# Optimization experiments

Hardware: AMD Instinct MI355X
Metric: run time of the kernel (lower is better)

## Reference

```python
import jax, jax.numpy as jnp
import numpy as np

B, T, P, N, D, H = 4, 8, 32, 64, 256, 8
M = 4 * D  # mlp hidden
EPS_LN = 1e-5


def _layernorm(x, g, b):
    mu = jnp.mean(x, axis=-1, keepdims=True)
    var = jnp.mean(jnp.square(x - mu), axis=-1, keepdims=True)
    return (x - mu) * jax.lax.rsqrt(var + EPS_LN) * g + b


def _attention(y, qkv_w, qkv_b, proj_w, proj_b, bias=None):
    # y: [Bb, Nn, D]; bias broadcastable to [Bb, H, Nn, Nn]
    Bb, Nn, Dd = y.shape
    hd = Dd // H
    qkv = (y @ qkv_w + qkv_b).reshape(Bb, Nn, 3, H, hd)
    qkv = jnp.transpose(qkv, (2, 0, 3, 1, 4))  # [3, Bb, H, Nn, hd]
    q, k, v = qkv[0], qkv[1], qkv[2]
    s = jnp.einsum('bhnd,bhmd->bhnm', q, k) * (hd ** -0.5)
    if bias is not None:
        s = s + bias
    a = jax.nn.softmax(s, axis=-1)
    o = jnp.einsum('bhnm,bhmd->bhnd', a, v)
    o = jnp.transpose(o, (0, 2, 1, 3)).reshape(Bb, Nn, Dd)
    return o @ proj_w + proj_b


def _mlp(y, fc1_w, fc1_b, fc2_w, fc2_b):
    h = jax.nn.gelu(y @ fc1_w + fc1_b, approximate=False)
    return h @ fc2_w + fc2_b


def setup_inputs():
    key = jax.random.key(0)
    ks = jax.random.split(key, 12)
    lin = lambda k, i, o: (jax.random.normal(k, (i, o), jnp.float32) * (i ** -0.5))
    inp = {}
    inp['x'] = jax.random.normal(ks[0], (B, T, P * N, D), jnp.float32)
    inp['mask'] = jax.random.bernoulli(ks[1], 0.8, (P, N)).astype(jnp.float32)
    inp['patch_adj'] = jax.random.uniform(ks[2], (N, N), jnp.float32, minval=0.01, maxval=1.0)
    inp['dn1_g'] = jnp.ones((D,)); inp['dn1_b'] = jnp.zeros((D,))
    inp['dn2_g'] = jnp.ones((D,)); inp['dn2_b'] = jnp.zeros((D,))
    inp['bn1_g'] = jnp.ones((D,)); inp['bn1_b'] = jnp.zeros((D,))
    inp['d_qkv_w'] = lin(ks[3], D, 3 * D); inp['d_qkv_b'] = jnp.zeros((3 * D,))
    inp['d_proj_w'] = lin(ks[4], D, D); inp['d_proj_b'] = jnp.zeros((D,))
    inp['d_fc1_w'] = lin(ks[5], D, M); inp['d_fc1_b'] = jnp.zeros((M,))
    inp['d_fc2_w'] = lin(ks[6], M, D); inp['d_fc2_b'] = jnp.zeros((D,))
    inp['b_qkv_w'] = lin(ks[7], D, 3 * D); inp['b_qkv_b'] = jnp.zeros((3 * D,))
    inp['b_proj_w'] = lin(ks[8], D, D); inp['b_proj_b'] = jnp.zeros((D,))
    inp['b_fc1_w'] = lin(ks[9], D, M); inp['b_fc1_b'] = jnp.zeros((M,))
    inp['b_fc2_w'] = lin(ks[10], M, D); inp['b_fc2_b'] = jnp.zeros((D,))
    return inp


def reference(x, mask, patch_adj, dn1_g, dn1_b, dn2_g, dn2_b, bn1_g, bn1_b,
              d_qkv_w, d_qkv_b, d_proj_w, d_proj_b, d_fc1_w, d_fc1_b, d_fc2_w, d_fc2_b,
              b_qkv_w, b_qkv_b, b_proj_w, b_proj_b, b_fc1_w, b_fc1_b, b_fc2_w, b_fc2_b):
    x5 = x.reshape(B, T, P, N, D)
    m = mask[None, None, :, :, None]  # [1,1,P,N,1]
    # --- depth (windowed) attention with log-adjacency bias ---
    y = _layernorm(x5, dn1_g, dn1_b).reshape(B * T * P, N, D)
    bias = jnp.log(patch_adj + 1e-6)[None, None, :, :]  # [1,1,N,N]
    y = _attention(y, d_qkv_w, d_qkv_b, d_proj_w, d_proj_b, bias=bias)
    x5 = x5 + y.reshape(B, T, P, N, D) * m
    # --- depth MLP ---
    y = _mlp(_layernorm(x5, dn2_g, dn2_b), d_fc1_w, d_fc1_b, d_fc2_w, d_fc2_b)
    x5 = x5 + y * m
    # --- masked mean-pool over nodes, breadth attention over patches ---
    z = (x5 * m).sum(axis=3) / jnp.clip(m.sum(axis=3), 1.0, None)  # [B,T,P,D]
    z = _layernorm(z.reshape(B * T, P, D), bn1_g, bn1_b)
    z = _attention(z, b_qkv_w, b_qkv_b, b_proj_w, b_proj_b)
    z = _mlp(z, b_fc1_w, b_fc1_b, b_fc2_w, b_fc2_b)
    x5 = x5 + z.reshape(B, T, P, D)[:, :, :, None, :]
    return x5.reshape(B, T, P * N, D)
```

## Files before the change

kernel.cpp:

```cpp
#include <hip/hip_runtime.h>
#include <hip/hip_bf16.h>
#include <math.h>

typedef __attribute__((ext_vector_type(8))) short short8;
typedef __attribute__((ext_vector_type(4))) float floatx4;

__device__ __forceinline__ float u2f(unsigned short u) {
    union { unsigned int i; float f; } x; x.i = ((unsigned int)u) << 16; return x.f;
}
__device__ __forceinline__ unsigned short f2u(float f) {
    union { float f; unsigned int i; } c; c.f = f;
    unsigned int r = c.i + 0x7FFF + ((c.i >> 16) & 1);
    return (unsigned short)(r >> 16);
}
__device__ __forceinline__ float gelu_exact(float x) {
    return 0.5f * x * (1.0f + erff(x * 0.7071067811865475f));
}

__global__ __launch_bounds__(256) void pack_weights_k(
    const float* __restrict__ W1, const float* __restrict__ W2,
    const float* __restrict__ Wqkv, const float* __restrict__ Wp,
    const float* __restrict__ bW1, const float* __restrict__ bW2,
    const float* __restrict__ bWqkv, const float* __restrict__ bWp,
    unsigned short* __restrict__ W1t, unsigned short* __restrict__ W2t,
    unsigned short* __restrict__ Wqkvt, unsigned short* __restrict__ Wpt,
    unsigned short* __restrict__ bW1t, unsigned short* __restrict__ bW2t,
    unsigned short* __restrict__ bWqkvt, unsigned short* __restrict__ bWpt)
{
    int b = blockIdx.x, t = threadIdx.x;
    if (b < 1024) {
        W1t[(size_t)b * 256 + t] = f2u(W1[(size_t)t * 1024 + b]);
    } else if (b < 1280) {
        int n = b - 1024;
        for (int it = 0; it < 4; ++it) {
            int k = it * 256 + t;
            W2t[(size_t)n * 1024 + k] = f2u(W2[(size_t)k * 256 + n]);
        }
    } else if (b < 2048) {
        int c = b - 1280;
        Wqkvt[(size_t)c * 256 + t] = f2u(Wqkv[(size_t)t * 768 + c]);
    } else if (b < 2304) {
        int c = b - 2048;
        Wpt[(size_t)c * 256 + t] = f2u(Wp[(size_t)t * 256 + c]);
    } else if (b < 3328) {
        int c = b - 2304;
        bW1t[(size_t)c * 256 + t] = f2u(bW1[(size_t)t * 1024 + c]);
    } else if (b < 3584) {
        int n = b - 3328;
        for (int it = 0; it < 4; ++it) {
            int k = it * 256 + t;
            bW2t[(size_t)n * 1024 + k] = f2u(bW2[(size_t)k * 256 + n]);
        }
    } else if (b < 4352) {
        int c = b - 3584;
        bWqkvt[(size_t)c * 256 + t] = f2u(bWqkv[(size_t)t * 768 + c]);
    } else {
        int c = b - 4352;
        bWpt[(size_t)c * 256 + t] = f2u(bWp[(size_t)t * 256 + c]);
    }
}

__global__ __launch_bounds__(256, 2) void attn_mfma_k(
    const float* __restrict__ x, const float* __restrict__ mask,
    const float* __restrict__ adj,
    const float* __restrict__ g1, const float* __restrict__ be1,
    const unsigned short* __restrict__ Wqkvt, const float* __restrict__ Bqkv,
    const unsigned short* __restrict__ Wpt, const float* __restrict__ Bp,
    float* __restrict__ out)
{
    __shared__ unsigned short Ybuf[64][264];
    __shared__ unsigned short qb[64][40];
    __shared__ unsigned short kb[64][40];
    __shared__ unsigned short Vt[32][72];
    __shared__ unsigned short Pb[64][72];
    __shared__ unsigned short Ob[64][40];

    int w = blockIdx.x, p = w & 31, t = threadIdx.x;
    int wave = t >> 6, lane = t & 63;
    int l15 = lane & 15, kw = lane >> 4;
    size_t base = (size_t)w * 16384;

    for (int it = 0; it < 16; ++it) {
        int r = it * 4 + wave;
        float vals[4]; float sum = 0.f, sq = 0.f;
#pragma unroll
        for (int k2 = 0; k2 < 4; ++k2) {
            float vv = x[base + (size_t)r * 256 + lane + 64 * k2];
            vals[k2] = vv; sum += vv; sq += vv * vv;
        }
        for (int o = 32; o > 0; o >>= 1) { sum += __shfl_xor(sum, o); sq += __shfl_xor(sq, o); }
        float mu = sum * (1.f / 256.f);
        float var = sq * (1.f / 256.f) - mu * mu;
        float rstd = rsqrtf(var + 1e-5f);
#pragma unroll
        for (int k2 = 0; k2 < 4; ++k2) {
            int c = lane + 64 * k2;
            Ybuf[r][c] = f2u((vals[k2] - mu) * rstd * g1[c] + be1[c]);
            out[base + (size_t)r * 256 + c] = vals[k2];
        }
    }
    __syncthreads();

    short8 ay[8];
#pragma unroll
    for (int ks = 0; ks < 8; ++ks)
        ay[ks] = *(const short8*)(&Ybuf[wave * 16 + l15][ks * 32 + kw * 8]);

    float ladj[4][4];
#pragma unroll
    for (int cf = 0; cf < 4; ++cf)
#pragma unroll
        for (int jj = 0; jj < 4; ++jj) {
            int r = wave * 16 + kw * 4 + jj;
            int c = cf * 16 + l15;
            ladj[cf][jj] = logf(adj[r * 64 + c] + 1e-6f);
        }

    floatx4 oacc[16];
#pragma unroll
    for (int cf = 0; cf < 16; ++cf) {
        float bb = Bp[cf * 16 + l15];
        oacc[cf] = (floatx4){bb, bb, bb, bb};
    }

    const float sc = 0.17677669529663689f;

    for (int h = 0; h < 8; ++h) {
        floatx4 qacc[6];
#pragma unroll
        for (int cf = 0; cf < 6; ++cf) {
            int gcol = (cf >> 1) * 256 + h * 32 + (cf & 1) * 16 + l15;
            float bb = Bqkv[gcol];
            qacc[cf] = (floatx4){bb, bb, bb, bb};
        }
#pragma unroll
        for (int ks = 0; ks < 8; ++ks) {
            short8 bw[6];
#pragma unroll
            for (int cf = 0; cf < 6; ++cf) {
                int gcol = (cf >> 1) * 256 + h * 32 + (cf & 1) * 16 + l15;
                bw[cf] = *(const short8*)(Wqkvt + (size_t)gcol * 256 + ks * 32 + kw * 8);
            }
#pragma unroll
            for (int cf = 0; cf < 6; ++cf)
                qacc[cf] = __builtin_amdgcn_mfma_f32_16x16x32_bf16(ay[ks], bw[cf], qacc[cf], 0, 0, 0);
        }
#pragma unroll
        for (int cf = 0; cf < 6; ++cf)
#pragma unroll
            for (int jj = 0; jj < 4; ++jj) {
                int r = wave * 16 + kw * 4 + jj;
                int d = (cf & 1) * 16 + l15;
                unsigned short ub = f2u(qacc[cf][jj]);
                if (cf < 2) qb[r][d] = ub;
                else if (cf < 4) kb[r][d] = ub;
                else Vt[d][r] = ub;
            }
        __syncthreads();

        short8 aq = *(const short8*)(&qb[wave * 16 + l15][kw * 8]);
        floatx4 sacc[4];
#pragma unroll
        for (int cf = 0; cf < 4; ++cf) {
            short8 bk = *(const short8*)(&kb[cf * 16 + l15][kw * 8]);
            sacc[cf] = __builtin_amdgcn_mfma_f32_16x16x32_bf16(aq, bk,
                        (floatx4){0.f, 0.f, 0.f, 0.f}, 0, 0, 0);
        }
#pragma unroll
        for (int jj = 0; jj < 4; ++jj) {
            float s0 = sacc[0][jj] * sc + ladj[0][jj];
            float s1 = sacc[1][jj] * sc + ladj[1][jj];
            float s2 = sacc[2][jj] * sc + ladj[2][jj];
            float s3 = sacc[3][jj] * sc + ladj[3][jj];
            float mx = fmaxf(fmaxf(s0, s1), fmaxf(s2, s3));
            mx = fmaxf(mx, __shfl_xor(mx, 1));
            mx = fmaxf(mx, __shfl_xor(mx, 2));
            mx = fmaxf(mx, __shfl_xor(mx, 4));
            mx = fmaxf(mx, __shfl_xor(mx, 8));
            float e0 = __expf(s0 - mx), e1 = __expf(s1 - mx);
            float e2 = __expf(s2 - mx), e3 = __expf(s3 - mx);
            float sum = e0 + e1 + e2 + e3;
            sum += __shfl_xor(sum, 1);
            sum += __shfl_xor(sum, 2);
            sum += __shfl_xor(sum, 4);
            sum += __shfl_xor(sum, 8);
            float inv = 1.f / sum;
            int r = wave * 16 + kw * 4 + jj;
            Pb[r][0 * 16 + l15] = f2u(e0 * inv);
            Pb[r][1 * 16 + l15] = f2u(e1 * inv);
            Pb[r][2 * 16 + l15] = f2u(e2 * inv);
            Pb[r][3 * 16 + l15] = f2u(e3 * inv);
        }
        __syncthreads();

        floatx4 oacc2[2];
#pragma unroll
        for (int cf2 = 0; cf2 < 2; ++cf2) oacc2[cf2] = (floatx4){0.f, 0.f, 0.f, 0.f};
#pragma unroll
        for (int ks = 0; ks < 2; ++ks) {
            short8 ap = *(const short8*)(&Pb[wave * 16 + l15][ks * 32 + kw * 8]);
#pragma unroll
            for (int cf2 = 0; cf2 < 2; ++cf2) {
                short8 bv = *(const short8*)(&Vt[cf2 * 16 + l15][ks * 32 + kw * 8]);
                oacc2[cf2] = __builtin_amdgcn_mfma_f32_16x16x32_bf16(ap, bv, oacc2[cf2], 0, 0, 0);
            }
        }
#pragma unroll
        for (int cf2 = 0; cf2 < 2; ++cf2)
#pragma unroll
            for (int jj = 0; jj < 4; ++jj)
                Ob[wave * 16 + kw * 4 + jj][cf2 * 16 + l15] = f2u(oacc2[cf2][jj]);
        __syncthreads();

        short8 ao = *(const short8*)(&Ob[wave * 16 + l15][kw * 8]);
#pragma unroll
        for (int cf = 0; cf < 16; ++cf) {
            short8 bw = *(const short8*)(Wpt + (size_t)(cf * 16 + l15) * 256 + h * 32 + kw * 8);
            oacc[cf] = __builtin_amdgcn_mfma_f32_16x16x32_bf16(ao, bw, oacc[cf], 0, 0, 0);
        }
        __syncthreads();
    }

#pragma unroll
    for (int jj = 0; jj < 4; ++jj) {
        int r = wave * 16 + kw * 4 + jj;
        float mv = mask[p * 64 + r];
#pragma unroll
        for (int cf = 0; cf < 16; ++cf) {
            size_t idx = base + (size_t)r * 256 + cf * 16 + l15;
            out[idx] += oacc[cf][jj] * mv;
        }
    }
}

__global__ __launch_bounds__(256) void mlp_mfma_k(
    const float* __restrict__ mask,
    const float* __restrict__ g2, const float* __restrict__ be2,
    const unsigned short* __restrict__ W1t, const float* __restrict__ B1,
    const unsigned short* __restrict__ W2t, const float* __restrict__ B2,
    float* __restrict__ out)
{
    __shared__ unsigned short Ybuf[64][264];
    __shared__ unsigned short Hbuf[64][72];
    __shared__ unsigned short Wbuf[10240];
    int w = blockIdx.x, p = w & 31, t = threadIdx.x;
    int wave = t >> 6, lane = t & 63;
    int l15 = lane & 15, kw = lane >> 4;
    size_t base = (size_t)w * 16384;

    for (int it = 0; it < 16; ++it) {
        int r = it * 4 + wave;
        float vals[4]; float sum = 0.f, sq = 0.f;
#pragma unroll
        for (int k2 = 0; k2 < 4; ++k2) {
            float vv = out[base + (size_t)r * 256 + lane + 64 * k2];
            vals[k2] = vv; sum += vv; sq += vv * vv;
        }
        for (int o = 32; o > 0; o >>= 1) { sum += __shfl_xor(sum, o); sq += __shfl_xor(sq, o); }
        float mu = sum * (1.f / 256.f);
        float var = sq * (1.f / 256.f) - mu * mu;
        float rstd = rsqrtf(var + 1e-5f);
#pragma unroll
        for (int k2 = 0; k2 < 4; ++k2) {
            int c = lane + 64 * k2;
            Ybuf[r][c] = f2u((vals[k2] - mu) * rstd * g2[c] + be2[c]);
        }
    }
    __syncthreads();

    floatx4 oacc[4][4];
#pragma unroll
    for (int m = 0; m < 4; ++m)
#pragma unroll
        for (int j = 0; j < 4; ++j) {
            float bb = B2[wave * 64 + j * 16 + l15];
            oacc[m][j] = (floatx4){bb, bb, bb, bb};
        }

    for (int pass = 0; pass < 16; ++pass) {
        floatx4 facc[4];
#pragma unroll
        for (int j = 0; j < 4; ++j) {
            float bb = B1[pass * 64 + j * 16 + l15];
            facc[j] = (floatx4){bb, bb, bb, bb};
        }
        {
            int nr = t >> 2, c = t & 3;
            *(short8*)(Wbuf + nr * 40 + c * 8) =
                *(const short8*)(W1t + (size_t)(pass * 64 + nr) * 256 + c * 8);
        }
        __syncthreads();
        for (int ks = 0; ks < 8; ++ks) {
            if (ks + 1 < 8) {
                int nr = t >> 2, c = t & 3;
                *(short8*)(Wbuf + ((ks + 1) & 1) * 2560 + nr * 40 + c * 8) =
                    *(const short8*)(W1t + (size_t)(pass * 64 + nr) * 256 + (ks + 1) * 32 + c * 8);
            }
            int hh = (ks & 1) * 2560;
            short8 a = *(const short8*)(&Ybuf[wave * 16 + l15][ks * 32 + kw * 8]);
            short8 bf[4];
#pragma unroll
            for (int j = 0; j < 4; ++j)
                bf[j] = *(const short8*)(Wbuf + hh + (j * 16 + l15) * 40 + kw * 8);
#pragma unroll
            for (int j = 0; j < 4; ++j)
                facc[j] = __builtin_amdgcn_mfma_f32_16x16x32_bf16(a, bf[j], facc[j], 0, 0, 0);
            __syncthreads();
        }
#pragma unroll
        for (int j = 0; j < 4; ++j)
#pragma unroll
            for (int jj = 0; jj < 4; ++jj)
                Hbuf[wave * 16 + kw * 4 + jj][j * 16 + l15] = f2u(gelu_exact(facc[j][jj]));
        __syncthreads();

        for (int ks2 = 0; ks2 < 2; ++ks2) {
            for (int it = 0; it < 4; ++it) {
                int idx = it * 256 + t;
                int nr = idx >> 2, c = idx & 3;
                *(short8*)(Wbuf + nr * 40 + c * 8) =
                    *(const short8*)(W2t + (size_t)nr * 1024 + pass * 64 + ks2 * 32 + c * 8);
            }
            __syncthreads();
            short8 af[4], bf[4];
#pragma unroll
            for (int m = 0; m < 4; ++m)
                af[m] = *(const short8*)(&Hbuf[m * 16 + l15][ks2 * 32 + kw * 8]);
#pragma unroll
            for (int j = 0; j < 4; ++j)
                bf[j] = *(const short8*)(Wbuf + (wave * 64 + j * 16 + l15) * 40 + kw * 8);
#pragma unroll
            for (int m = 0; m < 4; ++m)
#pragma unroll
                for (int j = 0; j < 4; ++j)
                    oacc[m][j] = __builtin_amdgcn_mfma_f32_16x16x32_bf16(af[m], bf[j], oacc[m][j], 0, 0, 0);
            __syncthreads();
        }
    }

#pragma unroll
    for (int m = 0; m < 4; ++m) {
#pragma unroll
        for (int jj = 0; jj < 4; ++jj) {
            int r = m * 16 + kw * 4 + jj;
            float mv = mask[p * 64 + r];
#pragma unroll
            for (int j = 0; j < 4; ++j) {
                size_t idx = base + (size_t)r * 256 + wave * 64 + j * 16 + l15;
                out[idx] += oacc[m][j][jj] * mv;
            }
        }
    }
}

__global__ __launch_bounds__(256) void pool_ln_k(
    const float* __restrict__ out, const float* __restrict__ mask,
    const float* __restrict__ gvec, const float* __restrict__ bvec,
    unsigned short* __restrict__ zln)
{
    __shared__ float red[2][4];
    int w = blockIdx.x, p = w & 31, t = threadIdx.x;
    int wave = t >> 6, lane = t & 63;
    size_t base = (size_t)w * 16384;
    float acc = 0.f, msum = 0.f;
    for (int nn = 0; nn < 64; ++nn) {
        float mv = mask[p * 64 + nn];
        msum += mv;
        acc += mv * out[base + (size_t)nn * 256 + t];
    }
    float z = acc / fmaxf(msum, 1.f);
    float s1 = z, s2 = z * z;
    for (int o = 32; o > 0; o >>= 1) { s1 += __shfl_xor(s1, o); s2 += __shfl_xor(s2, o); }
    if (lane == 0) { red[0][wave] = s1; red[1][wave] = s2; }
    __syncthreads();
    float t1 = red[0][0] + red[0][1] + red[0][2] + red[0][3];
    float t2 = red[1][0] + red[1][1] + red[1][2] + red[1][3];
    float mu = t1 * (1.f / 256.f);
    float var = t2 * (1.f / 256.f) - mu * mu;
    float rstd = rsqrtf(var + 1e-5f);
    zln[(size_t)w * 256 + t] = f2u((z - mu) * rstd * gvec[t] + bvec[t]);
}

__global__ __launch_bounds__(256) void zcompute_k(
    const unsigned short* __restrict__ zln,
    const unsigned short* __restrict__ bWqkvt, const float* __restrict__ Bqkv,
    const unsigned short* __restrict__ bWpt, const float* __restrict__ Bp,
    const unsigned short* __restrict__ bW1t, const float* __restrict__ B1,
    const unsigned short* __restrict__ bW2t, const float* __restrict__ B2,
    float* __restrict__ zout)
{
    __shared__ unsigned short Zbuf[32][264];
    __shared__ unsigned short Z2[32][264];
    __shared__ unsigned short qb[32][40], kb[32][40], Vt[32][40], Pb[32][40], Ob[32][40];
    __shared__ unsigned short Hbuf[32][72];
    int bt = blockIdx.x, t = threadIdx.x;
    int wave = t >> 6, lane = t & 63;
    int l15 = lane & 15, kw = lane >> 4;
    int rt = wave & 1, cq = wave >> 1;

    for (int i = t; i < 32 * 256; i += 256) {
        int r = i >> 8, c = i & 255;
        Zbuf[r][c] = zln[(size_t)bt * 8192 + i];
    }
    __syncthreads();

    short8 ay[8];
#pragma unroll
    for (int ks = 0; ks < 8; ++ks)
        ay[ks] = *(const short8*)(&Zbuf[rt * 16 + l15][ks * 32 + kw * 8]);

    floatx4 pacc[8];
#pragma unroll
    for (int cf = 0; cf < 8; ++cf) {
        float bb = Bp[cq * 128 + cf * 16 + l15];
        pacc[cf] = (floatx4){bb, bb, bb, bb};
    }
    const float sc = 0.17677669529663689f;

    for (int h = 0; h < 8; ++h) {
        floatx4 qacc[3];
#pragma unroll
        for (int cf = 0; cf < 3; ++cf) {
            int c96 = cq * 48 + cf * 16 + l15;
            int gcol = (c96 >> 5) * 256 + h * 32 + (c96 & 31);
            float bb = Bqkv[gcol];
            qacc[cf] = (floatx4){bb, bb, bb, bb};
        }
#pragma unroll
        for (int ks = 0; ks < 8; ++ks) {
#pragma unroll
            for (int cf = 0; cf < 3; ++cf) {
                int c96 = cq * 48 + cf * 16 + l15;
                int gcol = (c96 >> 5) * 256 + h * 32 + (c96 & 31);
                short8 bw = *(const short8*)(bWqkvt + (size_t)gcol * 256 + ks * 32 + kw * 8);
                qacc[cf] = __builtin_amdgcn_mfma_f32_16x16x32_bf16(ay[ks], bw, qacc[cf], 0, 0, 0);
            }
        }
#pragma unroll
        for (int cf = 0; cf < 3; ++cf) {
            int c96 = cq * 48 + cf * 16 + l15;
            int which = c96 >> 5, d = c96 & 31;
#pragma unroll
            for (int jj = 0; jj < 4; ++jj) {
                int r = rt * 16 + kw * 4 + jj;
                unsigned short ub = f2u(qacc[cf][jj]);
                if (which == 0) qb[r][d] = ub;
                else if (which == 1) kb[r][d] = ub;
                else Vt[d][r] = ub;
            }
        }
        __syncthreads();
        if (wave < 2) {
            short8 aq = *(const short8*)(&qb[wave * 16 + l15][kw * 8]);
            floatx4 sacc[2];
#pragma unroll
            for (int cf = 0; cf < 2; ++cf) {
                short8 bk = *(const short8*)(&kb[cf * 16 + l15][kw * 8]);
                sacc[cf] = __builtin_amdgcn_mfma_f32_16x16x32_bf16(aq, bk,
                            (floatx4){0.f, 0.f, 0.f, 0.f}, 0, 0, 0);
            }
#pragma unroll
            for (int jj = 0; jj < 4; ++jj) {
                float s0 = sacc[0][jj] * sc;
                float s1 = sacc[1][jj] * sc;
                float mx = fmaxf(s0, s1);
                mx = fmaxf(mx, __shfl_xor(mx, 1));
                mx = fmaxf(mx, __shfl_xor(mx, 2));
                mx = fmaxf(mx, __shfl_xor(mx, 4));
                mx = fmaxf(mx, __shfl_xor(mx, 8));
                float e0 = __expf(s0 - mx), e1 = __expf(s1 - mx);
                float sum = e0 + e1;
                sum += __shfl_xor(sum, 1);
                sum += __shfl_xor(sum, 2);
                sum += __shfl_xor(sum, 4);
                sum += __shfl_xor(sum, 8);
                float inv = 1.f / sum;
                int r = wave * 16 + kw * 4 + jj;
                Pb[r][l15] = f2u(e0 * inv);
                Pb[r][16 + l15] = f2u(e1 * inv);
            }
        }
        __syncthreads();
        {
            short8 ap = *(const short8*)(&Pb[rt * 16 + l15][kw * 8]);
            short8 bv = *(const short8*)(&Vt[cq * 16 + l15][kw * 8]);
            floatx4 oo = __builtin_amdgcn_mfma_f32_16x16x32_bf16(ap, bv,
                          (floatx4){0.f, 0.f, 0.f, 0.f}, 0, 0, 0);
#pragma unroll
            for (int jj = 0; jj < 4; ++jj)
                Ob[rt * 16 + kw * 4 + jj][cq * 16 + l15] = f2u(oo[jj]);
        }
        __syncthreads();
        {
            short8 ao = *(const short8*)(&Ob[rt * 16 + l15][kw * 8]);
#pragma unroll
            for (int cf = 0; cf < 8; ++cf) {
                int gcol = cq * 128 + cf * 16 + l15;
                short8 bw = *(const short8*)(bWpt + (size_t)gcol * 256 + h * 32 + kw * 8);
                pacc[cf] = __builtin_amdgcn_mfma_f32_16x16x32_bf16(ao, bw, pacc[cf], 0, 0, 0);
            }
        }
        __syncthreads();
    }
#pragma unroll
    for (int cf = 0; cf < 8; ++cf)
#pragma unroll
        for (int jj = 0; jj < 4; ++jj)
            Z2[rt * 16 + kw * 4 + jj][cq * 128 + cf * 16 + l15] = f2u(pacc[cf][jj]);
    __syncthreads();

    short8 az[8];
#pragma unroll
    for (int ks = 0; ks < 8; ++ks)
        az[ks] = *(const short8*)(&Z2[rt * 16 + l15][ks * 32 + kw * 8]);

    floatx4 oacc2[8];
#pragma unroll
    for (int cf = 0; cf < 8; ++cf) {
        float bb = B2[cq * 128 + cf * 16 + l15];
        oacc2[cf] = (floatx4){bb, bb, bb, bb};
    }
    for (int pass = 0; pass < 16; ++pass) {
        floatx4 facc[2];
#pragma unroll
        for (int cf = 0; cf < 2; ++cf) {
            int col = pass * 64 + cq * 32 + cf * 16 + l15;
            float bb = B1[col];
            facc[cf] = (floatx4){bb, bb, bb, bb};
        }
#pragma unroll
        for (int ks = 0; ks < 8; ++ks) {
#pragma unroll
            for (int cf = 0; cf < 2; ++cf) {
                int col = pass * 64 + cq * 32 + cf * 16 + l15;
                short8 bw = *(const short8*)(bW1t + (size_t)col * 256 + ks * 32 + kw * 8);
                facc[cf] = __builtin_amdgcn_mfma_f32_16x16x32_bf16(az[ks], bw, facc[cf], 0, 0, 0);
            }
        }
#pragma unroll
        for (int cf = 0; cf < 2; ++cf)
#pragma unroll
            for (int jj = 0; jj < 4; ++jj)
                Hbuf[rt * 16 + kw * 4 + jj][cq * 32 + cf * 16 + l15] = f2u(gelu_exact(facc[cf][jj]));
        __syncthreads();
#pragma unroll
        for (int ks = 0; ks < 2; ++ks) {
            short8 ah = *(const short8*)(&Hbuf[rt * 16 + l15][ks * 32 + kw * 8]);
#pragma unroll
            for (int cf = 0; cf < 8; ++cf) {
                int gcol = cq * 128 + cf * 16 + l15;
                short8 bw = *(const short8*)(bW2t + (size_t)gcol * 1024 + pass * 64 + ks * 32 + kw * 8);
                oacc2[cf] = __builtin_amdgcn_mfma_f32_16x16x32_bf16(ah, bw, oacc2[cf], 0, 0, 0);
            }
        }
        __syncthreads();
    }
#pragma unroll
    for (int cf = 0; cf < 8; ++cf)
#pragma unroll
        for (int jj = 0; jj < 4; ++jj) {
            int r = rt * 16 + kw * 4 + jj;
            int c = cq * 128 + cf * 16 + l15;
            zout[(size_t)bt * 8192 + r * 256 + c] = oacc2[cf][jj];
        }
}

__global__ __launch_bounds__(256) void zadd_k(
    const float* __restrict__ zout, float* __restrict__ out)
{
    int w = blockIdx.x, t = threadIdx.x;
    size_t base = (size_t)w * 16384;
    float zv = zout[(size_t)w * 256 + t];
    for (int nn = 0; nn < 64; ++nn)
        out[base + (size_t)nn * 256 + t] += zv;
}

extern "C" void kernel_launch(void* const* d_in, const int* in_sizes, int n_in,
                              void* d_out, int out_size, void* d_ws, size_t ws_size,
                              hipStream_t stream) {
    (void)in_sizes; (void)n_in; (void)out_size; (void)ws_size;
    const float* x        = (const float*)d_in[0];
    const float* mask     = (const float*)d_in[1];
    const float* adj      = (const float*)d_in[2];
    const float* dn1_g    = (const float*)d_in[3];
    const float* dn1_b    = (const float*)d_in[4];
    const float* dn2_g    = (const float*)d_in[5];
    const float* dn2_b    = (const float*)d_in[6];
    const float* bn1_g    = (const float*)d_in[7];
    const float* bn1_b    = (const float*)d_in[8];
    const float* d_qkv_w  = (const float*)d_in[9];
    const float* d_qkv_b  = (const float*)d_in[10];
    const float* d_proj_w = (const float*)d_in[11];
    const float* d_proj_b = (const float*)d_in[12];
    const float* d_fc1_w  = (const float*)d_in[13];
    const float* d_fc1_b  = (const float*)d_in[14];
    const float* d_fc2_w  = (const float*)d_in[15];
    const float* d_fc2_b  = (const float*)d_in[16];
    const float* b_qkv_w  = (const float*)d_in[17];
    const float* b_qkv_b  = (const float*)d_in[18];
    const float* b_proj_w = (const float*)d_in[19];
    const float* b_proj_b = (const float*)d_in[20];
    const float* b_fc1_w  = (const float*)d_in[21];
    const float* b_fc1_b  = (const float*)d_in[22];
    const float* b_fc2_w  = (const float*)d_in[23];
    const float* b_fc2_b  = (const float*)d_in[24];
    float* out = (float*)d_out;

    unsigned short* W1t    = (unsigned short*)d_ws;
    unsigned short* W2t    = W1t + 262144;
    unsigned short* Wqkvt  = W2t + 262144;
    unsigned short* Wpt    = Wqkvt + 196608;
    unsigned short* bW1t   = Wpt + 65536;
    unsigned short* bW2t   = bW1t + 262144;
    unsigned short* bWqkvt = bW2t + 262144;
    unsigned short* bWpt   = bWqkvt + 196608;
    unsigned short* zln    = bWpt + 65536;
    float* zout            = (float*)(zln + 262144);

    pack_weights_k<<<4608, 256, 0, stream>>>(d_fc1_w, d_fc2_w, d_qkv_w, d_proj_w,
                                             b_fc1_w, b_fc2_w, b_qkv_w, b_proj_w,
                                             W1t, W2t, Wqkvt, Wpt,
                                             bW1t, bW2t, bWqkvt, bWpt);
    attn_mfma_k<<<1024, 256, 0, stream>>>(x, mask, adj, dn1_g, dn1_b,
                                          Wqkvt, d_qkv_b, Wpt, d_proj_b, out);
    mlp_mfma_k<<<1024, 256, 0, stream>>>(mask, dn2_g, dn2_b,
                                         W1t, d_fc1_b, W2t, d_fc2_b, out);
    pool_ln_k<<<1024, 256, 0, stream>>>(out, mask, bn1_g, bn1_b, zln);
    zcompute_k<<<32, 256, 0, stream>>>(zln,
                                       bWqkvt, b_qkv_b, bWpt, b_proj_b,
                                       bW1t, b_fc1_b, bW2t, b_fc2_b, zout);
    zadd_k<<<1024, 256, 0, stream>>>(zout, out);
}
```

Before: 840.3 us.

## Fuse pooling into MLP epilogue, alias LDS buffers, raise occupancy, drop weight staging

Folds the masked node pooling into the MLP kernel's epilogue, writing per-block column sums, and moves the layernorm of pooled features into zcompute, eliminating the separate pool kernel and its re-read of the activations. Shared buffers in the attention and MLP kernels are aliased into one smaller region and launch bounds raised to three blocks per CU to increase occupancy. The MLP now reads weights directly from global/L2 instead of double-buffering them through LDS, removing several barriers. Some attention barriers are removed, relying on per-wave ownership of rows, which risks races if the remaining syncs are insufficient.

```diff
diff --git a/kernel.cpp b/kernel.cpp
--- a/kernel.cpp
+++ b/kernel.cpp
@@ -60,7 +60,7 @@
     }
 }
 
-__global__ __launch_bounds__(256, 2) void attn_mfma_k(
+__global__ __launch_bounds__(256, 3) void attn_mfma_k(
     const float* __restrict__ x, const float* __restrict__ mask,
     const float* __restrict__ adj,
     const float* __restrict__ g1, const float* __restrict__ be1,
@@ -68,12 +68,13 @@
     const unsigned short* __restrict__ Wpt, const float* __restrict__ Bp,
     float* __restrict__ out)
 {
-    __shared__ unsigned short Ybuf[64][264];
-    __shared__ unsigned short qb[64][40];
-    __shared__ unsigned short kb[64][40];
-    __shared__ unsigned short Vt[32][72];
-    __shared__ unsigned short Pb[64][72];
-    __shared__ unsigned short Ob[64][40];
+    __shared__ __align__(16) unsigned char smem[33792];
+    unsigned short (*Ybuf)[264] = (unsigned short (*)[264])smem;
+    unsigned short (*qb)[40]    = (unsigned short (*)[40])(smem);
+    unsigned short (*kb)[40]    = (unsigned short (*)[40])(smem + 5120);
+    unsigned short (*Vt)[72]    = (unsigned short (*)[72])(smem + 10240);
+    unsigned short (*Pb)[72]    = (unsigned short (*)[72])(smem + 14848);
+    unsigned short (*Ob)[40]    = (unsigned short (*)[40])(smem + 24064);
 
     int w = blockIdx.x, p = w & 31, t = threadIdx.x;
     int wave = t >> 6, lane = t & 63;
@@ -122,6 +123,7 @@
         float bb = Bp[cf * 16 + l15];
         oacc[cf] = (floatx4){bb, bb, bb, bb};
     }
+    __syncthreads();
 
     const float sc = 0.17677669529663689f;
 
@@ -191,7 +193,6 @@
             Pb[r][2 * 16 + l15] = f2u(e2 * inv);
             Pb[r][3 * 16 + l15] = f2u(e3 * inv);
         }
-        __syncthreads();
 
         floatx4 oacc2[2];
 #pragma unroll
@@ -218,7 +219,6 @@
             short8 bw = *(const short8*)(Wpt + (size_t)(cf * 16 + l15) * 256 + h * 32 + kw * 8);
             oacc[cf] = __builtin_amdgcn_mfma_f32_16x16x32_bf16(ao, bw, oacc[cf], 0, 0, 0);
         }
-        __syncthreads();
     }
 
 #pragma unroll
@@ -233,16 +233,17 @@
     }
 }
 
-__global__ __launch_bounds__(256) void mlp_mfma_k(
+__global__ __launch_bounds__(256, 3) void mlp_mfma_k(
     const float* __restrict__ mask,
     const float* __restrict__ g2, const float* __restrict__ be2,
     const unsigned short* __restrict__ W1t, const float* __restrict__ B1,
     const unsigned short* __restrict__ W2t, const float* __restrict__ B2,
-    float* __restrict__ out)
+    float* __restrict__ out, float* __restrict__ zsum)
 {
-    __shared__ unsigned short Ybuf[64][264];
-    __shared__ unsigned short Hbuf[64][72];
-    __shared__ unsigned short Wbuf[10240];
+    __shared__ __align__(16) unsigned char smem[33792];
+    unsigned short (*Ybuf)[264] = (unsigned short (*)[264])smem;
+    unsigned short (*Hbuf)[72]  = (unsigned short (*)[72])smem;
+
     int w = blockIdx.x, p = w & 31, t = threadIdx.x;
     int wave = t >> 6, lane = t & 63;
     int l15 = lane & 15, kw = lane >> 4;
@@ -268,6 +269,12 @@
     }
     __syncthreads();
 
+    short8 ay[8];
+#pragma unroll
+    for (int ks = 0; ks < 8; ++ks)
+        ay[ks] = *(const short8*)(&Ybuf[wave * 16 + l15][ks * 32 + kw * 8]);
+    __syncthreads();
+
     floatx4 oacc[4][4];
 #pragma unroll
     for (int m = 0; m < 4; ++m)
@@ -284,28 +291,15 @@
             float bb = B1[pass * 64 + j * 16 + l15];
             facc[j] = (floatx4){bb, bb, bb, bb};
         }
-        {
-            int nr = t >> 2, c = t & 3;
-            *(short8*)(Wbuf + nr * 40 + c * 8) =
-                *(const short8*)(W1t + (size_t)(pass * 64 + nr) * 256 + c * 8);
-        }
-        __syncthreads();
+#pragma unroll
         for (int ks = 0; ks < 8; ++ks) {
-            if (ks + 1 < 8) {
-                int nr = t >> 2, c = t & 3;
-                *(short8*)(Wbuf + ((ks + 1) & 1) * 2560 + nr * 40 + c * 8) =
-                    *(const short8*)(W1t + (size_t)(pass * 64 + nr) * 256 + (ks + 1) * 32 + c * 8);
-            }
-            int hh = (ks & 1) * 2560;
-            short8 a = *(const short8*)(&Ybuf[wave * 16 + l15][ks * 32 + kw * 8]);
             short8 bf[4];
 #pragma unroll
             for (int j = 0; j < 4; ++j)
-                bf[j] = *(const short8*)(Wbuf + hh + (j * 16 + l15) * 40 + kw * 8);
+                bf[j] = *(const short8*)(W1t + (size_t)(pass * 64 + j * 16 + l15) * 256 + ks * 32 + kw * 8);
 #pragma unroll
             for (int j = 0; j < 4; ++j)
-                facc[j] = __builtin_amdgcn_mfma_f32_16x16x32_bf16(a, bf[j], facc[j], 0, 0, 0);
-            __syncthreads();
+                facc[j] = __builtin_amdgcn_mfma_f32_16x16x32_bf16(ay[ks], bf[j], facc[j], 0, 0, 0);
         }
 #pragma unroll
         for (int j = 0; j < 4; ++j)
@@ -314,30 +308,25 @@
                 Hbuf[wave * 16 + kw * 4 + jj][j * 16 + l15] = f2u(gelu_exact(facc[j][jj]));
         __syncthreads();
 
+#pragma unroll
         for (int ks2 = 0; ks2 < 2; ++ks2) {
-            for (int it = 0; it < 4; ++it) {
-                int idx = it * 256 + t;
-                int nr = idx >> 2, c = idx & 3;
-                *(short8*)(Wbuf + nr * 40 + c * 8) =
-                    *(const short8*)(W2t + (size_t)nr * 1024 + pass * 64 + ks2 * 32 + c * 8);
-            }
-            __syncthreads();
             short8 af[4], bf[4];
 #pragma unroll
             for (int m = 0; m < 4; ++m)
                 af[m] = *(const short8*)(&Hbuf[m * 16 + l15][ks2 * 32 + kw * 8]);
 #pragma unroll
             for (int j = 0; j < 4; ++j)
-                bf[j] = *(const short8*)(Wbuf + (wave * 64 + j * 16 + l15) * 40 + kw * 8);
+                bf[j] = *(const short8*)(W2t + (size_t)(wave * 64 + j * 16 + l15) * 1024 + pass * 64 + ks2 * 32 + kw * 8);
 #pragma unroll
             for (int m = 0; m < 4; ++m)
 #pragma unroll
                 for (int j = 0; j < 4; ++j)
                     oacc[m][j] = __builtin_amdgcn_mfma_f32_16x16x32_bf16(af[m], bf[j], oacc[m][j], 0, 0, 0);
-            __syncthreads();
-        }
-    }
-
+        }
+        __syncthreads();
+    }
+
+    float zp[4] = {0.f, 0.f, 0.f, 0.f};
 #pragma unroll
     for (int m = 0; m < 4; ++m) {
 #pragma unroll
@@ -347,42 +336,27 @@
 #pragma unroll
             for (int j = 0; j < 4; ++j) {
                 size_t idx = base + (size_t)r * 256 + wave * 64 + j * 16 + l15;
-                out[idx] += oacc[m][j][jj] * mv;
-            }
-        }
-    }
-}
-
-__global__ __launch_bounds__(256) void pool_ln_k(
-    const float* __restrict__ out, const float* __restrict__ mask,
+                float nv = out[idx] + oacc[m][j][jj] * mv;
+                out[idx] = nv;
+                zp[j] += mv * nv;
+            }
+        }
+    }
+#pragma unroll
+    for (int j = 0; j < 4; ++j) {
+        zp[j] += __shfl_xor(zp[j], 16);
+        zp[j] += __shfl_xor(zp[j], 32);
+    }
+    if (kw == 0) {
+#pragma unroll
+        for (int j = 0; j < 4; ++j)
+            zsum[(size_t)w * 256 + wave * 64 + j * 16 + l15] = zp[j];
+    }
+}
+
+__global__ __launch_bounds__(256) void zcompute_k(
+    const float* __restrict__ zsum, const float* __restrict__ mask,
     const float* __restrict__ gvec, const float* __restrict__ bvec,
-    unsigned short* __restrict__ zln)
-{
-    __shared__ float red[2][4];
-    int w = blockIdx.x, p = w & 31, t = threadIdx.x;
-    int wave = t >> 6, lane = t & 63;
-    size_t base = (size_t)w * 16384;
-    float acc = 0.f, msum = 0.f;
-    for (int nn = 0; nn < 64; ++nn) {
-        float mv = mask[p * 64 + nn];
-        msum += mv;
-        acc += mv * out[base + (size_t)nn * 256 + t];
-    }
-    float z = acc / fmaxf(msum, 1.f);
-    float s1 = z, s2 = z * z;
-    for (int o = 32; o > 0; o >>= 1) { s1 += __shfl_xor(s1, o); s2 += __shfl_xor(s2, o); }
-    if (lane == 0) { red[0][wave] = s1; red[1][wave] = s2; }
-    __syncthreads();
-    float t1 = red[0][0] + red[0][1] + red[0][2] + red[0][3];
-    float t2 = red[1][0] + red[1][1] + red[1][2] + red[1][3];
-    float mu = t1 * (1.f / 256.f);
-    float var = t2 * (1.f / 256.f) - mu * mu;
-    float rstd = rsqrtf(var + 1e-5f);
-    zln[(size_t)w * 256 + t] = f2u((z - mu) * rstd * gvec[t] + bvec[t]);
-}
-
-__global__ __launch_bounds__(256) void zcompute_k(
-    const unsigned short* __restrict__ zln,
     const unsigned short* __restrict__ bWqkvt, const float* __restrict__ Bqkv,
     const unsigned short* __restrict__ bWpt, const float* __restrict__ Bp,
     const unsigned short* __restrict__ bW1t, const float* __restrict__ B1,
@@ -393,14 +367,37 @@
     __shared__ unsigned short Z2[32][264];
     __shared__ unsigned short qb[32][40], kb[32][40], Vt[32][40], Pb[32][40], Ob[32][40];
     __shared__ unsigned short Hbuf[32][72];
+    __shared__ float msh[32];
     int bt = blockIdx.x, t = threadIdx.x;
     int wave = t >> 6, lane = t & 63;
     int l15 = lane & 15, kw = lane >> 4;
     int rt = wave & 1, cq = wave >> 1;
 
-    for (int i = t; i < 32 * 256; i += 256) {
-        int r = i >> 8, c = i & 255;
-        Zbuf[r][c] = zln[(size_t)bt * 8192 + i];
+    if (t < 32) {
+        float s = 0.f;
+        for (int nn = 0; nn < 64; ++nn) s += mask[t * 64 + nn];
+        msh[t] = fmaxf(s, 1.f);
+    }
+    __syncthreads();
+
+    for (int it = 0; it < 8; ++it) {
+        int r = it * 4 + wave;
+        float inv_m = 1.f / msh[r];
+        float vals[4]; float sum = 0.f, sq = 0.f;
+#pragma unroll
+        for (int k2 = 0; k2 < 4; ++k2) {
+            float vv = zsum[(size_t)bt * 8192 + (size_t)r * 256 + lane + 64 * k2] * inv_m;
+            vals[k2] = vv; sum += vv; sq += vv * vv;
+        }
+        for (int o = 32; o > 0; o >>= 1) { sum += __shfl_xor(sum, o); sq += __shfl_xor(sq, o); }
+        float mu = sum * (1.f / 256.f);
+        float var = sq * (1.f / 256.f) - mu * mu;
+        float rstd = rsqrtf(var + 1e-5f);
+#pragma unroll
+        for (int k2 = 0; k2 < 4; ++k2) {
+            int c = lane + 64 * k2;
+            Zbuf[r][c] = f2u((vals[k2] - mu) * rstd * gvec[c] + bvec[c]);
+        }
     }
     __syncthreads();
 
@@ -614,8 +611,8 @@
     unsigned short* bW2t   = bW1t + 262144;
     unsigned short* bWqkvt = bW2t + 262144;
     unsigned short* bWpt   = bWqkvt + 196608;
-    unsigned short* zln    = bWpt + 65536;
-    float* zout            = (float*)(zln + 262144);
+    float* zsum            = (float*)(bWpt + 65536);
+    float* zout            = zsum + 262144;
 
     pack_weights_k<<<4608, 256, 0, stream>>>(d_fc1_w, d_fc2_w, d_qkv_w, d_proj_w,
                                              b_fc1_w, b_fc2_w, b_qkv_w, b_proj_w,
@@ -624,9 +621,8 @@
     attn_mfma_k<<<1024, 256, 0, stream>>>(x, mask, adj, dn1_g, dn1_b,
                                           Wqkvt, d_qkv_b, Wpt, d_proj_b, out);
     mlp_mfma_k<<<1024, 256, 0, stream>>>(mask, dn2_g, dn2_b,
-                                         W1t, d_fc1_b, W2t, d_fc2_b, out);
-    pool_ln_k<<<1024, 256, 0, stream>>>(out, mask, bn1_g, bn1_b, zln);
-    zcompute_k<<<32, 256, 0, stream>>>(zln,
+                                         W1t, d_fc1_b, W2t, d_fc2_b, out, zsum);
+    zcompute_k<<<32, 256, 0, stream>>>(zsum, mask, bn1_g, bn1_b,
                                        bWqkvt, b_qkv_b, bWpt, b_proj_b,
                                        bW1t, b_fc1_b, bW2t, b_fc2_b, zout);
     zadd_k<<<1024, 256, 0, stream>>>(zout, out);
```

New measurement: 1.079 ms. 1.28x slower.
